# Optimization experiments

Hardware: AMD Instinct MI355X
Metric: run time of the kernel (lower is better)

The kernel has to match this reference:

```python
import jax, jax.numpy as jnp
import numpy as np

B, T, V, D, L, FFM = 2, 2048, 50257, 1024, 8, 2


def setup_inputs() -> dict:
    key = jax.random.key(0)
    ks = jax.random.split(key, 10)
    s = 0.02
    return {
        "input_ids": jax.random.randint(ks[0], (B, T), 0, V),
        "embed": jax.random.normal(ks[1], (V, D), jnp.float32) * s,
        "norm1_w": jnp.ones((L, D), jnp.float32),
        "norm2_w": jnp.ones((L, D), jnp.float32),
        "a_diag": jax.random.uniform(ks[2], (L, D), jnp.float32, 0.5, 0.99),
        "W_in": jax.random.normal(ks[3], (L, D, D), jnp.float32) * s,
        "b_in": jnp.zeros((L, D), jnp.float32),
        "W_out": jax.random.normal(ks[4], (L, D, D), jnp.float32) * s,
        "ff_w1": jax.random.normal(ks[5], (L, D, FFM * D), jnp.float32) * s,
        "ff_b1": jnp.zeros((L, FFM * D), jnp.float32),
        "ff_w2": jax.random.normal(ks[6], (L, FFM * D, D), jnp.float32) * s,
        "ff_b2": jnp.zeros((L, D), jnp.float32),
        "final_norm_w": jnp.ones((D,), jnp.float32),
        "lm_head_w": jax.random.normal(ks[7], (V, D), jnp.float32) * s,
    }


def rmsnorm(x, w, eps=1e-6):
    return x * jax.lax.rsqrt(jnp.mean(x * x, axis=-1, keepdims=True) + eps) * w


def chaos_core(x, a, Win, bin_, Wout):
    pre = jnp.einsum('btd,de->bte', x, Win) + bin_  # precompute input drive (parallel)

    def step(s, p):
        s = jnp.tanh(a * s + p)
        return s, s

    s0 = jnp.zeros((x.shape[0], x.shape[-1]), x.dtype)
    _, hs = jax.lax.scan(step, s0, jnp.swapaxes(pre, 0, 1))  # (T, B, D)
    hs = jnp.swapaxes(hs, 0, 1)  # (B, T, D)
    return jnp.einsum('btd,de->bte', hs, Wout)


def reference(input_ids, embed, norm1_w, norm2_w, a_diag, W_in, b_in, W_out,
              ff_w1, ff_b1, ff_w2, ff_b2, final_norm_w, lm_head_w):
    x = embed[input_ids]  # (B, T, D)
    for i in range(L):
        # input_norm -> core -> residual
        x = x + chaos_core(rmsnorm(x, norm1_w[i]), a_diag[i], W_in[i], b_in[i], W_out[i])
        # ff_norm -> FeedForward (Linear -> SiLU -> Linear) -> residual
        h = rmsnorm(x, norm2_w[i])
        h = jax.nn.silu(jnp.einsum('btd,df->btf', h, ff_w1[i]) + ff_b1[i])
        x = x + jnp.einsum('btf,fd->btd', h, ff_w2[i]) + ff_b2[i]
    x = rmsnorm(x, final_norm_w)
    return jnp.einsum('btd,vd->btv', x, lm_head_w)  # logits (B, T, V)
```

## Files before the change

### kernel.cpp

```cpp
#include <hip/hip_runtime.h>

typedef unsigned short u16;
typedef __bf16 bf16x8 __attribute__((ext_vector_type(8)));
typedef float f32x4 __attribute__((ext_vector_type(4)));
typedef unsigned short u16x4 __attribute__((ext_vector_type(4)));

__device__ __forceinline__ u16 f2bf(float f) {
  union { float f; unsigned int u; } v; v.f = f;
  return (u16)((v.u + 0x7FFFu + ((v.u >> 16) & 1u)) >> 16);
}

__device__ __forceinline__ void gload16(const void* g, void* l) {
  __builtin_amdgcn_global_load_lds(
      (const __attribute__((address_space(1))) unsigned int*)g,
      (__attribute__((address_space(3))) unsigned int*)l, 16, 0, 0);
}


__global__ void transpose_cast_kernel(const float* __restrict__ W, u16* __restrict__ WT,
                                      int R, int C) {
  __shared__ float tile[32][33];
  const int tx = threadIdx.x, ty = threadIdx.y;
  const size_t zoff = (size_t)blockIdx.z * R * C;
  const int c0 = blockIdx.x * 32, r0 = blockIdx.y * 32;
#pragma unroll
  for (int k = 0; k < 32; k += 8)
    tile[ty + k][tx] = W[zoff + (size_t)(r0 + ty + k) * C + (c0 + tx)];
  __syncthreads();
#pragma unroll
  for (int k = 0; k < 32; k += 8)
    WT[zoff + (size_t)(c0 + ty + k) * R + (r0 + tx)] = f2bf(tile[tx][ty + k]);
}

__global__ void lm_cast_kernel(const float* __restrict__ lm, u16* __restrict__ out) {
  const int row = blockIdx.x;
  const int t = threadIdx.x;
  u16x4 o = {0, 0, 0, 0};
  if (row < 50257) {
    float4 v = *(const float4*)(lm + (size_t)row * 1024 + t * 4);
    o.x = f2bf(v.x); o.y = f2bf(v.y); o.z = f2bf(v.z); o.w = f2bf(v.w);
  }
  *(u16x4*)(out + (size_t)row * 1024 + t * 4) = o;
}

__global__ void embed_kernel(const int* __restrict__ ids, const float* __restrict__ embed,
                             float* __restrict__ x) {
  const int row = blockIdx.x;
  const int id = ids[row];
  const int t = threadIdx.x;
  *(float4*)(x + (size_t)row * 1024 + t * 4) =
      *(const float4*)(embed + (size_t)id * 1024 + t * 4);
}

__global__ void rmsnorm_kernel(const float* __restrict__ x, const float* __restrict__ w,
                               u16* __restrict__ out) {
  const int row = blockIdx.x, tid = threadIdx.x;
  const float* xr = x + (size_t)row * 1024;
  float4 v = *(const float4*)(xr + tid * 4);
  float ss = v.x * v.x + v.y * v.y + v.z * v.z + v.w * v.w;
#pragma unroll
  for (int off = 32; off; off >>= 1) ss += __shfl_xor(ss, off);
  __shared__ float red[4];
  if ((tid & 63) == 0) red[tid >> 6] = ss;
  __syncthreads();
  const float tot = red[0] + red[1] + red[2] + red[3];
  const float r = rsqrtf(tot * (1.0f / 1024.0f) + 1e-6f);
  float4 wv = *(const float4*)(w + tid * 4);
  u16x4 o;
  o.x = f2bf(v.x * r * wv.x); o.y = f2bf(v.y * r * wv.y);
  o.z = f2bf(v.z * r * wv.z); o.w = f2bf(v.w * r * wv.w);
  *(u16x4*)(out + (size_t)row * 1024 + tid * 4) = o;
}

__device__ __forceinline__ void scan_load(const float* __restrict__ p, int tb,
                                          float A2, float (&buf)[8]) {
#pragma unroll
  for (int j = 0; j < 8; j++)
    buf[j] = fmaf(p[(size_t)(tb + j) * 1024], 2.8853900817779268f, A2);
}

__device__ __forceinline__ void scan_comp(float (&buf)[8], float m2A2, float& r,
                                          u16* __restrict__ o, int tb) {
#pragma unroll
  for (int j = 0; j < 8; j++) {
    float z = fmaf(m2A2, r, buf[j]);
    float e = __builtin_amdgcn_exp2f(z);
    r = __builtin_amdgcn_rcpf(1.0f + e);
    o[(size_t)(tb + j) * 1024] = f2bf(fmaf(-2.0f, r, 1.0f));
  }
}

__global__ __launch_bounds__(256) void scan_kernel(const float* __restrict__ pre,
                                                   const float* __restrict__ a_diag,
                                                   u16* __restrict__ hs) {
  const int T = 2048;
  const int idx = blockIdx.x * 256 + threadIdx.x;
  const int b = idx >> 10, d = idx & 1023;
  const float* p = pre + (size_t)b * T * 1024 + d;
  u16* o = hs + (size_t)b * T * 1024 + d;
  const float A2 = a_diag[d] * 2.8853900817779268f;
  const float m2A2 = -2.0f * A2;
  float r = 0.5f;
  float b0[8], b1[8], b2[8], b3[8];
  scan_load(p, 0, A2, b0); scan_load(p, 8, A2, b1);
  scan_load(p, 16, A2, b2); scan_load(p, 24, A2, b3);
  for (int t0 = 0; t0 < T; t0 += 32) {
    scan_comp(b0, m2A2, r, o, t0);
    if (t0 + 32 < T) scan_load(p, t0 + 32, A2, b0);
    scan_comp(b1, m2A2, r, o, t0 + 8);
    if (t0 + 32 < T) scan_load(p, t0 + 40, A2, b1);
    scan_comp(b2, m2A2, r, o, t0 + 16);
    if (t0 + 32 < T) scan_load(p, t0 + 48, A2, b2);
    scan_comp(b3, m2A2, r, o, t0 + 24);
    if (t0 + 32 < T) scan_load(p, t0 + 56, A2, b3);
  }
}

template <int EPI>
__global__ __launch_bounds__(256) void gemm_nt(
    const u16* __restrict__ A, const u16* __restrict__ Bw,
    const float* __restrict__ bias, float* Cf, u16* __restrict__ Cb,
    int M, int N, int K, int ldc, int Nreal) {
  __shared__ char lds[32768];
  const int tid = threadIdx.x;
  const int lane = tid & 63;
  const int wid = tid >> 6;
  const int wm = wid >> 1, wn = wid & 1;
  int tm, tn;
  if (EPI == 3) {
    const int bid = blockIdx.x;
    const int xcd = bid & 7;
    const int i = bid >> 3;
    tm = (xcd * 4 + (i & 3)) * 128;
    tn = (i >> 2) * 128;
  } else {
    tm = blockIdx.y * 128;
    tn = blockIdx.x * 128;
  }

  const size_t sA = (size_t)K * 2;
  const int r0 = tid >> 2;
  const int slot = (tid & 3) ^ ((tid >> 3) & 3);
  const char* pA = (const char*)A + (size_t)(tm + r0) * sA + (slot << 4);
  const char* pB = (const char*)Bw + (size_t)(tn + r0) * sA + (slot << 4);
  const size_t rowskip = 64 * sA;

  const int lr = lane & 15;
  const int rdoff = ((lane >> 4) << 4) ^ (((lr >> 1) & 3) << 4);
  int aOff[4], bOff[4];
#pragma unroll
  for (int m = 0; m < 4; m++) aOff[m] = (wm * 64 + m * 16 + lr) * 64 + rdoff;
#pragma unroll
  for (int n = 0; n < 4; n++) bOff[n] = 8192 + (wn * 64 + n * 16 + lr) * 64 + rdoff;

  f32x4 acc[4][4] = {};

  {
    char* dA = lds + tid * 16;
    gload16(pA, dA);
    gload16(pA + rowskip, dA + 4096);
    gload16(pB, dA + 8192);
    gload16(pB + rowskip, dA + 12288);
  }
  __syncthreads();

  int cur = 0;
  for (int k0 = 0; k0 < K; k0 += 32) {
    if (k0 + 32 < K) {
      const size_t kb = (size_t)(k0 + 32) * 2;
      char* dA = lds + (cur ^ 1) * 16384 + tid * 16;
      gload16(pA + kb, dA);
      gload16(pA + rowskip + kb, dA + 4096);
      gload16(pB + kb, dA + 8192);
      gload16(pB + rowskip + kb, dA + 12288);
    }
    const char* base = lds + cur * 16384;
    bf16x8 af[4], bfr[4];
#pragma unroll
    for (int m = 0; m < 4; m++) af[m] = *(const bf16x8*)(base + aOff[m]);
#pragma unroll
    for (int n = 0; n < 4; n++) bfr[n] = *(const bf16x8*)(base + bOff[n]);
#pragma unroll
    for (int m = 0; m < 4; m++)
#pragma unroll
      for (int n = 0; n < 4; n++)
        acc[m][n] =
            __builtin_amdgcn_mfma_f32_16x16x32_bf16(af[m], bfr[n], acc[m][n], 0, 0, 0);
    __syncthreads();
    cur ^= 1;
  }

  const int crow = tm + wm * 64 + ((lane >> 4) << 2);
  const int ccol = tn + wn * 64 + lr;
#pragma unroll
  for (int m = 0; m < 4; m++) {
#pragma unroll
    for (int n = 0; n < 4; n++) {
      const int cg = ccol + n * 16;
      float bb = 0.0f;
      if (EPI != 3) bb = bias ? bias[cg] : 0.0f;
#pragma unroll
      for (int j = 0; j < 4; j++) {
        const size_t off = (size_t)(crow + m * 16 + j) * ldc + cg;
        const float v = acc[m][n][j] + bb;
        if (EPI == 0) {
          Cf[off] = v;
        } else if (EPI == 1) {
          Cf[off] += v;
        } else if (EPI == 2) {
          const float sg = __builtin_amdgcn_rcpf(
              1.0f + __builtin_amdgcn_exp2f(-1.4426950408889634f * v));
          Cb[off] = f2bf(v * sg);
        } else {
          if (cg < Nreal) Cf[off] = v;
        }
      }
    }
  }
}

extern "C" void kernel_launch(void* const* d_in, const int* in_sizes, int n_in,
                              void* d_out, int out_size, void* d_ws, size_t ws_size,
                              hipStream_t stream) {
  const int T = 2048, D = 1024, V = 50257, L = 8;
  const int M = 2 * T;
  const int Vpad = 50304;

  const int* ids = (const int*)d_in[0];
  const float* embed = (const float*)d_in[1];
  const float* norm1_w = (const float*)d_in[2];
  const float* norm2_w = (const float*)d_in[3];
  const float* a_diag = (const float*)d_in[4];
  const float* W_in = (const float*)d_in[5];
  const float* b_in = (const float*)d_in[6];
  const float* W_out = (const float*)d_in[7];
  const float* ff_w1 = (const float*)d_in[8];
  const float* ff_b1 = (const float*)d_in[9];
  const float* ff_w2 = (const float*)d_in[10];
  const float* ff_b2 = (const float*)d_in[11];
  const float* final_norm_w = (const float*)d_in[12];
  const float* lm_head_w = (const float*)d_in[13];

  char* w = (char*)d_ws;
  float* x = (float*)w;      w += (size_t)M * D * 4;
  u16* h = (u16*)w;          w += (size_t)M * D * 2;
  float* pre = (float*)w;    w += (size_t)M * D * 4;
  u16* hs = (u16*)w;         w += (size_t)M * D * 2;
  u16* hff = (u16*)w;        w += (size_t)M * 2 * D * 2;
  u16* WinT = (u16*)w;       w += (size_t)L * D * D * 2;
  u16* WoutT = (u16*)w;      w += (size_t)L * D * D * 2;
  u16* ffw1T = (u16*)w;      w += (size_t)L * 2 * D * D * 2;
  u16* ffw2T = (u16*)w;      w += (size_t)L * 2 * D * D * 2;
  u16* lmpad = (u16*)w;      w += (size_t)Vpad * D * 2;

  lm_cast_kernel<<<Vpad, 256, 0, stream>>>(lm_head_w, lmpad);
  transpose_cast_kernel<<<dim3(32, 32, L), dim3(32, 8), 0, stream>>>(W_in, WinT, D, D);
  transpose_cast_kernel<<<dim3(32, 32, L), dim3(32, 8), 0, stream>>>(W_out, WoutT, D, D);
  transpose_cast_kernel<<<dim3(64, 32, L), dim3(32, 8), 0, stream>>>(ff_w1, ffw1T, D, 2 * D);
  transpose_cast_kernel<<<dim3(32, 64, L), dim3(32, 8), 0, stream>>>(ff_w2, ffw2T, 2 * D, D);

  embed_kernel<<<M, 256, 0, stream>>>(ids, embed, x);

  for (int l = 0; l < L; l++) {
    rmsnorm_kernel<<<M, 256, 0, stream>>>(x, norm1_w + (size_t)l * D, h);
    gemm_nt<0><<<dim3(8, 32), 256, 0, stream>>>(
        h, WinT + (size_t)l * D * D, b_in + (size_t)l * D, pre, nullptr,
        M, D, D, D, D);
    scan_kernel<<<8, 256, 0, stream>>>(pre, a_diag + (size_t)l * D, hs);
    gemm_nt<1><<<dim3(8, 32), 256, 0, stream>>>(
        hs, WoutT + (size_t)l * D * D, nullptr, x, nullptr,
        M, D, D, D, D);
    rmsnorm_kernel<<<M, 256, 0, stream>>>(x, norm2_w + (size_t)l * D, h);
    gemm_nt<2><<<dim3(16, 32), 256, 0, stream>>>(
        h, ffw1T + (size_t)l * 2 * D * D, ff_b1 + (size_t)l * 2 * D, nullptr, hff,
        M, 2 * D, D, 2 * D, 2 * D);
    gemm_nt<1><<<dim3(8, 32), 256, 0, stream>>>(
        hff, ffw2T + (size_t)l * 2 * D * D, ff_b2 + (size_t)l * D, x, nullptr,
        M, D, 2 * D, D, D);
  }

  rmsnorm_kernel<<<M, 256, 0, stream>>>(x, final_norm_w, h);
  gemm_nt<3><<<dim3(12576), 256, 0, stream>>>(
      h, lmpad, nullptr, (float*)d_out, nullptr,
      M, Vpad, D, V, V);
}
```

Before: 3.212 ms.

## Use 64x64 tiles with K=64 steps for per-layer GEMMs to fill CUs

Per-layer GEMMs move from 128x128 tiles to a new 64x64-tile kernel that loads 64-wide K slices with an XOR swizzle. This raises the block count from 256 to 1024 (2048 for FF1), so all CUs on the MI355X are occupied. The LM-head GEMM is split into its own specialized kernel. In exchange, each block reuses less data and generates more global and LDS traffic per FLOP.

```diff
diff --git a/kernel.cpp b/kernel.cpp
--- a/kernel.cpp
+++ b/kernel.cpp
@@ -117,26 +117,115 @@
 }
 
 template <int EPI>
-__global__ __launch_bounds__(256) void gemm_nt(
+__global__ __launch_bounds__(256) void gemm64(
     const u16* __restrict__ A, const u16* __restrict__ Bw,
     const float* __restrict__ bias, float* Cf, u16* __restrict__ Cb,
-    int M, int N, int K, int ldc, int Nreal) {
+    int M, int N, int K, int ldc) {
   __shared__ char lds[32768];
   const int tid = threadIdx.x;
   const int lane = tid & 63;
   const int wid = tid >> 6;
   const int wm = wid >> 1, wn = wid & 1;
-  int tm, tn;
-  if (EPI == 3) {
-    const int bid = blockIdx.x;
-    const int xcd = bid & 7;
-    const int i = bid >> 3;
-    tm = (xcd * 4 + (i & 3)) * 128;
-    tn = (i >> 2) * 128;
-  } else {
-    tm = blockIdx.y * 128;
-    tn = blockIdx.x * 128;
-  }
+  const int tm = blockIdx.y * 64, tn = blockIdx.x * 64;
+
+  const size_t sA = (size_t)K * 2;
+  const int srow = tid >> 3;
+  const int ss = (tid & 7) ^ (srow & 7);
+  const char* pA = (const char*)A + (size_t)(tm + srow) * sA + (ss << 4);
+  const char* pB = (const char*)Bw + (size_t)(tn + srow) * sA + (ss << 4);
+  const size_t pskip = 32 * sA;
+
+  const int lr = lane & 15;
+  int aOff[2][2], bOff[2][2];
+#pragma unroll
+  for (int m = 0; m < 2; m++)
+#pragma unroll
+    for (int h = 0; h < 2; h++) {
+      const int ra = wm * 32 + m * 16 + lr;
+      aOff[m][h] = ra * 128 + ((((lane >> 4) + 4 * h) ^ (ra & 7)) << 4);
+      const int rb = wn * 32 + m * 16 + lr;
+      bOff[m][h] = 8192 + rb * 128 + ((((lane >> 4) + 4 * h) ^ (rb & 7)) << 4);
+    }
+
+  f32x4 acc[2][2] = {};
+
+  {
+    char* d = lds + tid * 16;
+    gload16(pA, d);
+    gload16(pA + pskip, d + 4096);
+    gload16(pB, d + 8192);
+    gload16(pB + pskip, d + 12288);
+  }
+  __syncthreads();
+
+  int cur = 0;
+  for (int k0 = 0; k0 < K; k0 += 64) {
+    if (k0 + 64 < K) {
+      const size_t kb = (size_t)(k0 + 64) * 2;
+      char* d = lds + (cur ^ 1) * 16384 + tid * 16;
+      gload16(pA + kb, d);
+      gload16(pA + pskip + kb, d + 4096);
+      gload16(pB + kb, d + 8192);
+      gload16(pB + pskip + kb, d + 12288);
+    }
+    const char* base = lds + cur * 16384;
+    bf16x8 aF[2][2], bF[2][2];
+#pragma unroll
+    for (int m = 0; m < 2; m++)
+#pragma unroll
+      for (int h = 0; h < 2; h++) {
+        aF[m][h] = *(const bf16x8*)(base + aOff[m][h]);
+        bF[m][h] = *(const bf16x8*)(base + bOff[m][h]);
+      }
+#pragma unroll
+    for (int h = 0; h < 2; h++)
+#pragma unroll
+      for (int m = 0; m < 2; m++)
+#pragma unroll
+        for (int n = 0; n < 2; n++)
+          acc[m][n] = __builtin_amdgcn_mfma_f32_16x16x32_bf16(aF[m][h], bF[n][h],
+                                                              acc[m][n], 0, 0, 0);
+    __syncthreads();
+    cur ^= 1;
+  }
+
+  const int crow = tm + wm * 32 + ((lane >> 4) << 2);
+  const int ccol = tn + wn * 32 + lr;
+#pragma unroll
+  for (int m = 0; m < 2; m++) {
+#pragma unroll
+    for (int n = 0; n < 2; n++) {
+      const int cg = ccol + n * 16;
+      const float bb = bias ? bias[cg] : 0.0f;
+#pragma unroll
+      for (int j = 0; j < 4; j++) {
+        const size_t off = (size_t)(crow + m * 16 + j) * ldc + cg;
+        const float v = acc[m][n][j] + bb;
+        if (EPI == 0) {
+          Cf[off] = v;
+        } else if (EPI == 1) {
+          Cf[off] += v;
+        } else {
+          const float sg = __builtin_amdgcn_rcpf(
+              1.0f + __builtin_amdgcn_exp2f(-1.4426950408889634f * v));
+          Cb[off] = f2bf(v * sg);
+        }
+      }
+    }
+  }
+}
+
+__global__ __launch_bounds__(256) void gemm_lm(
+    const u16* __restrict__ A, const u16* __restrict__ Bw,
+    float* __restrict__ Cf, int K, int ldc, int Nreal) {
+  __shared__ char lds[32768];
+  const int tid = threadIdx.x;
+  const int lane = tid & 63;
+  const int wid = tid >> 6;
+  const int wm = wid >> 1, wn = wid & 1;
+  const int bid = blockIdx.x;
+  const int tm = (((bid & 7) << 2) + ((bid >> 3) & 3)) * 128;
+  const int tn = (bid >> 5) * 128;
 
   const size_t sA = (size_t)K * 2;
   const int r0 = tid >> 2;
@@ -197,23 +286,10 @@
 #pragma unroll
     for (int n = 0; n < 4; n++) {
       const int cg = ccol + n * 16;
-      float bb = 0.0f;
-      if (EPI != 3) bb = bias ? bias[cg] : 0.0f;
 #pragma unroll
       for (int j = 0; j < 4; j++) {
-        const size_t off = (size_t)(crow + m * 16 + j) * ldc + cg;
-        const float v = acc[m][n][j] + bb;
-        if (EPI == 0) {
-          Cf[off] = v;
-        } else if (EPI == 1) {
-          Cf[off] += v;
-        } else if (EPI == 2) {
-          const float sg = __builtin_amdgcn_rcpf(
-              1.0f + __builtin_amdgcn_exp2f(-1.4426950408889634f * v));
-          Cb[off] = f2bf(v * sg);
-        } else {
-          if (cg < Nreal) Cf[off] = v;
-        }
+        if (cg < Nreal)
+          Cf[(size_t)(crow + m * 16 + j) * ldc + cg] = acc[m][n][j];
       }
     }
   }
@@ -263,24 +339,22 @@
 
   for (int l = 0; l < L; l++) {
     rmsnorm_kernel<<<M, 256, 0, stream>>>(x, norm1_w + (size_t)l * D, h);
-    gemm_nt<0><<<dim3(8, 32), 256, 0, stream>>>(
+    gemm64<0><<<dim3(16, 64), 256, 0, stream>>>(
         h, WinT + (size_t)l * D * D, b_in + (size_t)l * D, pre, nullptr,
-        M, D, D, D, D);
+        M, D, D, D);
     scan_kernel<<<8, 256, 0, stream>>>(pre, a_diag + (size_t)l * D, hs);
-    gemm_nt<1><<<dim3(8, 32), 256, 0, stream>>>(
+    gemm64<1><<<dim3(16, 64), 256, 0, stream>>>(
         hs, WoutT + (size_t)l * D * D, nullptr, x, nullptr,
-        M, D, D, D, D);
+        M, D, D, D);
     rmsnorm_kernel<<<M, 256, 0, stream>>>(x, norm2_w + (size_t)l * D, h);
-    gemm_nt<2><<<dim3(16, 32), 256, 0, stream>>>(
+    gemm64<2><<<dim3(32, 64), 256, 0, stream>>>(
         h, ffw1T + (size_t)l * 2 * D * D, ff_b1 + (size_t)l * 2 * D, nullptr, hff,
-        M, 2 * D, D, 2 * D, 2 * D);
-    gemm_nt<1><<<dim3(8, 32), 256, 0, stream>>>(
+        M, 2 * D, D, 2 * D);
+    gemm64<1><<<dim3(16, 64), 256, 0, stream>>>(
         hff, ffw2T + (size_t)l * 2 * D * D, ff_b2 + (size_t)l * D, x, nullptr,
-        M, D, 2 * D, D, D);
+        M, D, 2 * D, D);
   }
 
   rmsnorm_kernel<<<M, 256, 0, stream>>>(x, final_norm_w, h);
-  gemm_nt<3><<<dim3(12576), 256, 0, stream>>>(
-      h, lmpad, nullptr, (float*)d_out, nullptr,
-      M, Vpad, D, V, V);
-}
+  gemm_lm<<<dim3(12576), 256, 0, stream>>>(h, lmpad, (float*)d_out, D, V, V);
+}
```

New measurement: 2.784 ms. 13.3% less time.
